# Kernel optimization log

Measured on AMD Instinct MI355X. Metric: run time of the kernel, lower is better.

## Reference

```python
import math
import jax, jax.numpy as jnp
import numpy as np

P = 8; K = 9; RC = 8; FC = 768; TOPK = 2
THR = 0.2; TEMP = 0.08; DIL = 5; MIX = 0.65; OPEN = 5


def _build_bank():
    axis = np.linspace(-1.0, 1.0, K, dtype=np.float32)
    yy, xx = np.meshgrid(axis, axis, indexing='ij')
    Ls = [0.45, 0.75, 1.05]; Ws = [0.14, 0.2, 0.28]
    kernels, oris, lens, wids = [], [], [], []
    for i in range(P):
        ang = 2.0 * math.pi * i / P
        L = Ls[i % 3]; W = Ws[(i // 3) % 3]
        xr = xx * math.cos(ang) + yy * math.sin(ang)
        yr = -xx * math.sin(ang) + yy * math.cos(ang)
        taper = (1.0 - np.clip(np.abs(xr) / L, 0.0, 1.0)) ** 1.5
        core = np.exp(-0.5 * ((xr / L) ** 2 + (yr / W) ** 2))
        ridge = taper * core * np.clip(1.0 - (yr / W) ** 2, 0.0, None)
        k = ridge - ridge.mean()
        k = k / max(np.abs(k).sum(), 1e-6)
        kernels.append(k.astype(np.float32)); oris.append(ang); lens.append(L); wids.append(W)
    return (jnp.asarray(np.stack(kernels)[:, None]),
            jnp.asarray(np.array(oris, np.float32)),
            jnp.asarray(np.array(lens, np.float32)),
            jnp.asarray(np.array(wids, np.float32)))


def _conv(x, w, b, pad):
    y = jax.lax.conv_general_dilated(x, w, (1, 1), [(pad, pad), (pad, pad)],
                                     dimension_numbers=('NCHW', 'OIHW', 'NCHW'))
    return y + b[None, :, None, None]


def _avg3(x):  # torch avg_pool2d k=3,s=1,p=1 with count_include_pad=True -> sum/9
    s = jax.lax.reduce_window(x, 0.0, jax.lax.add, (1, 1, 3, 3), (1, 1, 1, 1),
                              [(0, 0), (0, 0), (1, 1), (1, 1)])
    return s / 9.0


def _maxp(x, k):
    p = k // 2
    return jax.lax.reduce_window(x, -jnp.inf, jax.lax.max, (1, 1, k, k), (1, 1, 1, 1),
                                 [(0, 0), (0, 0), (p, p), (p, p)])


def _binary_open(mask, k):
    eroded = 1.0 - _maxp(1.0 - mask, k)
    return jnp.clip(_maxp(eroded, k), 0.0, 1.0)


def _normalize(t):
    mn = t.min(axis=(-2, -1), keepdims=True)
    mx = t.max(axis=(-2, -1), keepdims=True)
    return (t - mn) / jnp.maximum(mx - mn, 1e-6)


def _gelu(x):
    return jax.nn.gelu(x, approximate=False)


def _forward(feature_map, theta, length, width, curvature, alpha, objectness,
             prototype_logits, fp1_w, fp1_b, fp2_w, fp2_b, pm1_w, pm1_b,
             pm2_w, pm2_b, proto_delta):
    bank, ori, la, wa = _build_bank()
    carrier = _gelu(_conv(_gelu(_conv(feature_map, fp1_w, fp1_b, 0)), fp2_w, fp2_b, 1))
    carrier_mean = carrier.mean(axis=1, keepdims=True)
    carrier_hp = carrier_mean - _avg3(carrier_mean)
    kernels = bank + 0.05 * proto_delta
    responses = jax.lax.conv_general_dilated(carrier_hp, kernels, (1, 1),
                                             [(K // 2, K // 2)] * 2,
                                             dimension_numbers=('NCHW', 'OIHW', 'NCHW'))
    theta_angle = jnp.tanh(theta) * math.pi  # [B,1,H,W]
    theta_score = jnp.cos(theta_angle - ori[None, :, None, None])
    length_value = jax.nn.sigmoid(length) * 0.85 + 0.25
    width_value = jax.nn.sigmoid(width) * 0.22 + 0.08
    length_score = -(length_value - la[None, :, None, None]) ** 2 / 0.08
    width_score = -(width_value - wa[None, :, None, None]) ** 2 / 0.01
    bias = prototype_logits + 1.25 * theta_score + length_score + width_score
    pw = jax.nn.softmax(bias, axis=1)  # [B,P,H,W]
    # per-pixel top-k prototype selection
    pwt = jnp.moveaxis(pw, 1, -1)  # [B,H,W,P]
    vals, idx = jax.lax.top_k(pwt, TOPK)
    sparse = (jax.nn.one_hot(idx, P, dtype=pw.dtype) * vals[..., None]).sum(axis=-2)
    sparse = sparse / jnp.maximum(sparse.sum(axis=-1, keepdims=True), 1e-6)
    pw = jnp.moveaxis(sparse, -1, 1)
    alpha_map = jax.nn.sigmoid(alpha)
    objectness_map = jax.nn.sigmoid(objectness)
    curvature_map = jnp.tanh(curvature)
    ss = (responses * pw).sum(axis=1, keepdims=True)
    ss = ss - _avg3(ss)
    density = jnp.abs(carrier).mean(axis=1, keepdims=True)
    density = density / jnp.maximum(density.mean(axis=(2, 3), keepdims=True), 1e-6)
    dx = jnp.cos(theta_angle); dy = jnp.sin(theta_angle)
    blob = _avg3(objectness_map)
    # support gating (enabled, hard-mask + opening)
    carrier_support = _normalize(_avg3(jnp.abs(carrier_hp)))
    density_support = _normalize(density)
    ev = MIX * carrier_support + (1.0 - MIX) * density_support
    gate = jax.nn.sigmoid((ev - THR) / TEMP)
    gate = _maxp(gate, DIL)
    mask = (ev >= THR).astype(feature_map.dtype)
    mask = _binary_open(mask, OPEN)
    mask = _maxp(mask, DIL)
    gate = gate * mask
    blob = blob * jax.lax.stop_gradient(gate)
    stroke_gate = alpha_map * blob * (0.7 + 0.3 * jnp.clip(density, 0.0, 2.0))
    ss = stroke_gate * ss * (1.0 + 0.15 * curvature_map)
    feats = jnp.concatenate([carrier * ss, ss, dx * ss, dy * ss, curvature_map * ss], axis=1)  # [B,RC+4,H,W]
    h = _gelu(_conv(feats, pm1_w, pm1_b, 0))
    return _conv(h, pm2_w, pm2_b, 0)  # [B,FC,H,W]


def setup_inputs() -> dict:
    key = jax.random.key(0)
    ks = jax.random.split(key, 16)
    B, H, W = 8, 64, 64
    n = lambda k, s: jax.random.normal(k, s, dtype=jnp.float32)
    return {
        'feature_map': n(ks[0], (B, FC, H, W)),
        'theta': n(ks[1], (B, 1, H, W)),
        'length': n(ks[2], (B, 1, H, W)),
        'width': n(ks[3], (B, 1, H, W)),
        'curvature': n(ks[4], (B, 1, H, W)),
        'alpha': n(ks[5], (B, 1, H, W)),
        'objectness': n(ks[6], (B, 1, H, W)),
        'prototype_logits': n(ks[7], (B, P, H, W)),
        'fp1_w': n(ks[8], (RC, FC, 1, 1)) * 0.02,
        'fp1_b': jnp.zeros((RC,), jnp.float32),
        'fp2_w': n(ks[9], (RC, RC, 3, 3)) * 0.05,
        'fp2_b': jnp.zeros((RC,), jnp.float32),
        'pm1_w': n(ks[10], (RC, RC + 4, 1, 1)) * 0.05,
        'pm1_b': jnp.zeros((RC,), jnp.float32),
        'pm2_w': n(ks[11], (FC, RC, 1, 1)) * 0.05,
        'pm2_b': jnp.zeros((FC,), jnp.float32),
        'proto_delta': n(ks[12], (P, 1, K, K)) * 0.02,
    }


def reference(feature_map, theta, length, width, curvature, alpha, objectness,
              prototype_logits, fp1_w, fp1_b, fp2_w, fp2_b, pm1_w, pm1_b,
              pm2_w, pm2_b, proto_delta):
    return _forward(feature_map, theta, length, width, curvature, alpha, objectness,
                    prototype_logits, fp1_w, fp1_b, fp2_w, fp2_b, pm1_w, pm1_b,
                    pm2_w, pm2_b, proto_delta)
```

## Files before the change

kernel.cpp:

```cpp
#include <hip/hip_runtime.h>
#include <math.h>

#define PI_F 3.14159265358979323846f

__device__ __forceinline__ float gelu_f(float x){ return 0.5f*x*(1.0f+erff(x*0.7071067811865475f)); }
__device__ __forceinline__ float sigm_f(float x){ return 1.0f/(1.0f+expf(-x)); }


__global__ void __launch_bounds__(256) k_conv1(const float* __restrict__ fm,
                        const float* __restrict__ w1, float* __restrict__ part){
    int chunk = blockIdx.x;
    int g = blockIdx.y;
    int tid = threadIdx.x;
    __shared__ float wl[96*8];
    for (int i=tid;i<96*8;i+=256){ int c=i>>3, co=i&7; wl[i]=w1[co*768 + g*96 + c]; }
    __syncthreads();
    int b = chunk>>2;
    int q0 = ((chunk&3)<<8) + tid;
    const float4* fm4 = (const float4*)fm;
    float4 acc[8];
    #pragma unroll
    for(int co=0;co<8;co++) acc[co]=make_float4(0.f,0.f,0.f,0.f);
    int basec = b*768 + g*96;
    for(int c=0;c<96;c++){
        float4 x = fm4[(size_t)(basec+c)*1024 + q0];
        #pragma unroll
        for(int co=0;co<8;co++){
            float wv = wl[(c<<3)+co];
            acc[co].x += wv*x.x; acc[co].y += wv*x.y; acc[co].z += wv*x.z; acc[co].w += wv*x.w;
        }
    }
    float4* p4 = (float4*)part;
    int gq = (b<<10) + q0;
    #pragma unroll
    for(int co=0;co<8;co++) p4[(size_t)(g*8+co)*8192 + gq] = acc[co];
}

__global__ void __launch_bounds__(256) k_bank(const float* __restrict__ pd,
                                              float* __restrict__ klg){
    __shared__ float ridge[648];
    __shared__ float pmS[8], pdenS[8];
    int tid = threadIdx.x;
    for(int t=tid;t<648;t+=256){
        int p=t/81, idx=t-p*81;
        int i=idx/9, j=idx-i*9;
        float ay=-1.f+0.25f*(float)i;
        float ax=-1.f+0.25f*(float)j;
        float ang=2.f*PI_F*(float)p*0.125f;
        const float Ls[3]={0.45f,0.75f,1.05f};
        const float Ws[3]={0.14f,0.20f,0.28f};
        float L=Ls[p%3], Wd=Ws[(p/3)%3];
        float cs=cosf(ang), sn=sinf(ang);
        float xr=ax*cs+ay*sn;
        float yr=-ax*sn+ay*cs;
        float tp=1.f-fminf(fabsf(xr)/L,1.f);
        float taper=powf(tp,1.5f);
        float core=expf(-0.5f*((xr/L)*(xr/L)+(yr/Wd)*(yr/Wd)));
        ridge[t]=taper*core*fmaxf(1.f-(yr/Wd)*(yr/Wd),0.f);
    }
    __syncthreads();
    {
        int p=tid>>5, k=tid&31;
        float s=0.f;
        for(int e=k;e<81;e+=32) s+=ridge[p*81+e];
        for(int off=16;off>0;off>>=1) s+=__shfl_down(s,off,32);
        if(k==0) pmS[p]=s*(1.f/81.f);
    }
    __syncthreads();
    {
        int p=tid>>5, k=tid&31;
        float m=pmS[p];
        float s=0.f;
        for(int e=k;e<81;e+=32) s+=fabsf(ridge[p*81+e]-m);
        for(int off=16;off>0;off>>=1) s+=__shfl_down(s,off,32);
        if(k==0) pdenS[p]=fmaxf(s,1e-6f);
    }
    __syncthreads();
    for(int t=tid;t<648;t+=256){
        int p=t/81;
        klg[t]=(ridge[t]-pmS[p])/pdenS[p]+0.05f*pd[t];
    }
}

__global__ void __launch_bounds__(256) k_comb(float* __restrict__ part,
                                              const float* __restrict__ b1){
    int idx = blockIdx.x*256 + threadIdx.x;
    int co = idx>>13, rem = idx&8191;
    float4* p4 = (float4*)part;
    float4 s = make_float4(0.f,0.f,0.f,0.f);
    #pragma unroll
    for(int g=0;g<8;g++){
        float4 v = p4[(size_t)((g<<3)+co)*8192 + rem];
        s.x+=v.x; s.y+=v.y; s.z+=v.z; s.w+=v.w;
    }
    float bb=b1[co];
    s.x=gelu_f(s.x+bb); s.y=gelu_f(s.y+bb); s.z=gelu_f(s.z+bb); s.w=gelu_f(s.w+bb);
    p4[(size_t)co*8192 + rem] = s;
}

__global__ void __launch_bounds__(256) k_conv2(const float* __restrict__ t1,
    const float* __restrict__ w2, const float* __restrict__ b2,
    float* __restrict__ carrier, float* __restrict__ cm, float* __restrict__ absc,
    float* __restrict__ bpart){
    __shared__ float t1T[8][256];
    __shared__ float w2s[576];
    __shared__ float sumS[2][128];
    __shared__ float saS[2][128];
    __shared__ float rS[256], rMn[256], rMx[256];
    int tid=threadIdx.x, bl=blockIdx.x;
    int b=bl>>5, band=bl&31, y0=band<<1;
    for(int i=tid;i<576;i+=256) w2s[i]=w2[i];
    {
        int r=tid>>6, x=tid&63;
        int gy=y0-1+r;
        bool ok = (gy>=0 && gy<64);
        int base = (b<<12)+(gy<<6)+x;
        #pragma unroll
        for(int co=0;co<8;co++)
            t1T[co][tid] = ok ? t1[co*32768 + base] : 0.f;
    }
    __syncthreads();
    int px=tid&127, half=tid>>7;
    int ly=px>>6, x=px&63, gy=y0+ly;
    float acc[4];
    #pragma unroll
    for(int qq=0;qq<4;qq++) acc[qq]=b2[half*4+qq];
    for(int ci=0;ci<8;ci++){
        #pragma unroll
        for(int dy=-1;dy<=1;dy++){
            int tr=ly+1+dy;
            #pragma unroll
            for(int dx=-1;dx<=1;dx++){
                int xx=x+dx;
                float v=(xx>=0&&xx<64)?t1T[ci][tr*64+xx]:0.f;
                int ti=(dy+1)*3+(dx+1);
                #pragma unroll
                for(int qq=0;qq<4;qq++) acc[qq]+=v*w2s[((half*4+qq)*8+ci)*9+ti];
            }
        }
    }
    float s4=0.f, sa4=0.f;
    #pragma unroll
    for(int qq=0;qq<4;qq++){
        float cv=gelu_f(acc[qq]);
        carrier[((size_t)((b<<3)+half*4+qq)<<12)+(gy<<6)+x]=cv;
        s4+=cv; sa4+=fabsf(cv);
    }
    sumS[half][px]=s4; saS[half][px]=sa4;
    __syncthreads();
    float aS=0.f, aMn=1e30f, aMx=-1e30f;
    if(half==0){
        float cmv=(sumS[0][px]+sumS[1][px])*0.125f;
        float av =(saS[0][px]+saS[1][px])*0.125f;
        int gp=(b<<12)+(gy<<6)+x;
        cm[gp]=cmv;
        absc[gp]=av;
        aS=av; aMn=av; aMx=av;
    }
    rS[tid]=aS; rMn[tid]=aMn; rMx[tid]=aMx;
    __syncthreads();
    for(int st=128;st>0;st>>=1){
        if(tid<st){
            rS[tid]+=rS[tid+st];
            rMn[tid]=fminf(rMn[tid],rMn[tid+st]);
            rMx[tid]=fmaxf(rMx[tid],rMx[tid+st]);
        }
        __syncthreads();
    }
    if(tid==0){
        bpart[bl*8+0]=rS[0];
        bpart[bl*8+3]=rMn[0];
        bpart[bl*8+4]=rMx[0];
    }
}

__global__ void __launch_bounds__(256) k_resp(const float* __restrict__ cm,
    const float* __restrict__ klg, const float* __restrict__ theta,
    const float* __restrict__ length, const float* __restrict__ width,
    const float* __restrict__ plog,
    float* __restrict__ csraw, float* __restrict__ ss0, float* __restrict__ bpart){
    __shared__ float cmT[768];
    __shared__ float chpT[640];
    __shared__ float klS[648];
    __shared__ float mg[128][8];
    __shared__ float rMn[256], rMx[256];
    int tid=threadIdx.x, bl=blockIdx.x;
    int b=bl>>5, band=bl&31, y0=band<<1;
    for(int i=tid;i<648;i+=256) klS[i]=klg[i];
    for(int j=tid;j<768;j+=256){
        int r=j>>6, x=j&63;
        int gy=y0-5+r;
        cmT[j]=(gy>=0&&gy<64)?cm[(b<<12)+(gy<<6)+x]:0.f;
    }
    __syncthreads();
    for(int j=tid;j<640;j+=256){
        int rh=j>>6, x=j&63;
        int gy=y0-4+rh;
        float v=0.f;
        if(gy>=0&&gy<64){
            float s=0.f;
            #pragma unroll
            for(int dy=-1;dy<=1;dy++){
                #pragma unroll
                for(int dx=-1;dx<=1;dx++){
                    int xx=x+dx;
                    if(xx>=0&&xx<64) s+=cmT[(rh+1+dy)*64+xx];
                }
            }
            v=cmT[(rh+1)*64+x]-s*(1.f/9.f);
        }
        chpT[j]=v;
    }
    __syncthreads();
    int px=tid&127, half=tid>>7;
    int ly=px>>6, x=px&63, gy=y0+ly;
    int gp=(b<<12)+(gy<<6)+x;
    float acc[4];
    #pragma unroll
    for(int qq=0;qq<4;qq++) acc[qq]=0.f;
    float cs=0.f;
    for(int dy=-4;dy<=4;dy++){
        int lr=ly+dy+4;
        for(int dx=-4;dx<=4;dx++){
            int xx=x+dx;
            float v=(xx>=0&&xx<64)?chpT[lr*64+xx]:0.f;
            int ti=(dy+4)*9+(dx+4);
            #pragma unroll
            for(int qq=0;qq<4;qq++) acc[qq]+=v*klS[(half*4+qq)*81+ti];
            if(half==0 && dy>=-1&&dy<=1&&dx>=-1&&dx<=1) cs+=fabsf(v);
        }
    }
    float ta=tanhf(theta[gp])*PI_F;
    float lv=sigm_f(length[gp])*0.85f+0.25f;
    float wv=sigm_f(width[gp])*0.22f+0.08f;
    const float Ls[3]={0.45f,0.75f,1.05f};
    const float Ws[3]={0.14f,0.20f,0.28f};
    int pp=(gy<<6)+x;
    float m1=-1e30f,m2=-1e30f,r1v=0.f,r2v=0.f;
    #pragma unroll
    for(int qq=0;qq<4;qq++){
        int q=half*4+qq;
        float ang=2.f*PI_F*(float)q*0.125f;
        float la=Ls[q%3], wa=Ws[(q/3)%3];
        float bias=plog[((size_t)((b<<3)+q)<<12)+pp]
                 +1.25f*cosf(ta-ang)
                 -(lv-la)*(lv-la)*(1.f/0.08f)
                 -(wv-wa)*(wv-wa)*(1.f/0.01f);
        if(bias>m1){m2=m1;r2v=r1v;m1=bias;r1v=acc[qq];}
        else if(bias>m2){m2=bias;r2v=acc[qq];}
    }
    mg[px][half*4+0]=m1; mg[px][half*4+1]=r1v;
    mg[px][half*4+2]=m2; mg[px][half*4+3]=r2v;
    __syncthreads();
    float cMn=1e30f, cMx=-1e30f;
    if(half==0){
        float m1a=mg[px][0], r1a=mg[px][1], m2a=mg[px][2], r2a=mg[px][3];
        float m1b=mg[px][4], r1b=mg[px][5], m2b=mg[px][6], r2b=mg[px][7];
        float M1,R1,M2,R2;
        if(m1b>m1a){ M1=m1b;R1=r1b; if(m2b>m1a){M2=m2b;R2=r2b;} else {M2=m1a;R2=r1a;} }
        else       { M1=m1a;R1=r1a; if(m1b>m2a){M2=m1b;R2=r1b;} else {M2=m2a;R2=r2a;} }
        float e2=expf(M2-M1);
        float inv=1.0f/(1.0f+e2);
        ss0[gp]=R1*inv + R2*e2*inv;
        float csv=cs*(1.f/9.f);
        csraw[gp]=csv;
        cMn=csv; cMx=csv;
    }
    rMn[tid]=cMn; rMx[tid]=cMx;
    __syncthreads();
    for(int st=128;st>0;st>>=1){
        if(tid<st){
            rMn[tid]=fminf(rMn[tid],rMn[tid+st]);
            rMx[tid]=fmaxf(rMx[tid],rMx[tid+st]);
        }
        __syncthreads();
    }
    if(tid==0){
        bpart[bl*8+1]=rMn[0];
        bpart[bl*8+2]=rMx[0];
    }
}

__global__ void __launch_bounds__(1024) k_gate(const float* __restrict__ csraw,
    const float* __restrict__ absc, const float* __restrict__ objn,
    const float* __restrict__ alpha, const float* __restrict__ bpart,
    float* __restrict__ sg){
    __shared__ float A[4096], Bs[4096], Cs[4096];
    __shared__ float red5[5];
    int b=blockIdx.x, tid=threadIdx.x;
    if(tid==0){
        float sm=0.f, cmn=1e30f, cmx=-1e30f, amn=1e30f, amx=-1e30f;
        for(int j=0;j<32;j++){
            const float* bp=&bpart[(b*32+j)*8];
            sm+=bp[0];
            cmn=fminf(cmn,bp[1]); cmx=fmaxf(cmx,bp[2]);
            amn=fminf(amn,bp[3]); amx=fmaxf(amx,bp[4]);
        }
        float den=fmaxf(sm*(1.0f/4096.0f),1e-6f);
        red5[0]=den; red5[1]=cmn; red5[2]=cmx; red5[3]=amn/den; red5[4]=amx/den;
    }
    __syncthreads();
    float den=red5[0], cmn=red5[1], cmx=red5[2], dmn=red5[3], dmx=red5[4];
    float cinv = 1.0f/fmaxf(cmx-cmn,1e-6f);
    float dinv = 1.0f/fmaxf(dmx-dmn,1e-6f);
    for(int k=0;k<4;k++){
        int p=tid+k*1024;
        float cs=(csraw[(b<<12)+p]-cmn)*cinv;
        float d = absc[(b<<12)+p]/den;
        float ds=(d-dmn)*dinv;
        float ev = 0.65f*cs + 0.35f*ds;
        A[p]=ev;
        Bs[p]=sigm_f((ev-0.2f)*(1.0f/0.08f));
    }
    __syncthreads();
    for(int k=0;k<4;k++){
        int p=tid+k*1024; int y=p>>6,x=p&63;
        float m=-1e30f;
        for(int dy=-2;dy<=2;dy++){int yy=y+dy; if(yy<0||yy>=64)continue;
            for(int dx=-2;dx<=2;dx++){int xx=x+dx; if(xx<0||xx>=64)continue;
                m=fmaxf(m,Bs[(yy<<6)+xx]);}}
        Cs[p]=m;
    }
    __syncthreads();
    for(int k=0;k<4;k++){
        int p=tid+k*1024; int y=p>>6,x=p&63;
        float m=1.f;
        for(int dy=-2;dy<=2;dy++){int yy=y+dy; if(yy<0||yy>=64)continue;
            for(int dx=-2;dx<=2;dx++){int xx=x+dx; if(xx<0||xx>=64)continue;
                if (A[(yy<<6)+xx] < 0.2f) m=0.f;}}
        Bs[p]=m;
    }
    __syncthreads();
    for(int k=0;k<4;k++){
        int p=tid+k*1024; int y=p>>6,x=p&63;
        float m=-1e30f;
        for(int dy=-2;dy<=2;dy++){int yy=y+dy; if(yy<0||yy>=64)continue;
            for(int dx=-2;dx<=2;dx++){int xx=x+dx; if(xx<0||xx>=64)continue;
                m=fmaxf(m,Bs[(yy<<6)+xx]);}}
        A[p]=m;
    }
    __syncthreads();
    for(int k=0;k<4;k++){
        int p=tid+k*1024; int y=p>>6,x=p&63;
        float m=-1e30f;
        for(int dy=-2;dy<=2;dy++){int yy=y+dy; if(yy<0||yy>=64)continue;
            for(int dx=-2;dx<=2;dx++){int xx=x+dx; if(xx<0||xx>=64)continue;
                m=fmaxf(m,A[(yy<<6)+xx]);}}
        Bs[p]=m;
    }
    __syncthreads();
    for(int k=0;k<4;k++){
        int p=tid+k*1024;
        A[p]=sigm_f(objn[(b<<12)+p]);
    }
    __syncthreads();
    for(int k=0;k<4;k++){
        int p=tid+k*1024; int y=p>>6,x=p&63;
        float s=0.f;
        for(int dy=-1;dy<=1;dy++){int yy=y+dy; if(yy<0||yy>=64)continue;
            for(int dx=-1;dx<=1;dx++){int xx=x+dx; if(xx<0||xx>=64)continue;
                s += A[(yy<<6)+xx];}}
        float blob = s*(1.0f/9.0f);
        float gate = Cs[p]*Bs[p];
        float d = absc[(b<<12)+p]/den;
        float sgv = sigm_f(alpha[(b<<12)+p]) * blob * gate * (0.7f+0.3f*fminf(fmaxf(d,0.f),2.f));
        sg[(b<<12)+p] = sgv;
    }
}

__global__ void __launch_bounds__(256) k_out(const float* __restrict__ ss0,
    const float* __restrict__ sg, const float* __restrict__ theta,
    const float* __restrict__ curv, const float* __restrict__ carrier,
    const float* __restrict__ w3, const float* __restrict__ b3,
    const float* __restrict__ w4, const float* __restrict__ b4,
    float* __restrict__ out){
    __shared__ float hS[8][128];
    __shared__ float w4s[768*8];
    __shared__ float b4s[768];
    __shared__ float wl[96];
    __shared__ float bl3[8];
    int tid=threadIdx.x;
    int bln=blockIdx.x;
    for(int i=tid;i<6144;i+=256) w4s[i]=w4[i];
    for(int i=tid;i<768;i+=256) b4s[i]=b4[i];
    if(tid<96) wl[tid]=w3[tid];
    if(tid<8) bl3[tid]=b3[tid];
    __syncthreads();

    if(tid<128){
        int gp=bln*128+tid;
        int b=gp>>12, p=gp&4095, y=p>>6, x=p&63;
        const float* base = ss0 + (b<<12);
        float s=0.f;
        for(int dy=-1;dy<=1;dy++){int yy=y+dy; if(yy<0||yy>=64)continue;
            for(int dx=-1;dx<=1;dx++){int xx=x+dx;if(xx<0||xx>=64)continue;
                s+=base[(yy<<6)+xx];}}
        float ss1 = base[p]-s*(1.0f/9.0f);
        float cu = tanhf(curv[gp]);
        float ssv = sg[gp]*ss1*(1.0f+0.15f*cu);
        float ta = tanhf(theta[gp])*PI_F;
        float dxv=cosf(ta), dyv=sinf(ta);
        float car[8];
        #pragma unroll
        for(int ci=0;ci<8;ci++) car[ci]=carrier[((size_t)((b<<3)+ci)<<12)+p];
        #pragma unroll
        for(int co=0;co<8;co++){
            const float* w=&wl[co*12];
            float t = w[8] + w[9]*dxv + w[10]*dyv + w[11]*cu;
            #pragma unroll
            for(int ci=0;ci<8;ci++) t += w[ci]*car[ci];
            hS[co][tid] = gelu_f(bl3[co] + ssv*t);
        }
    }
    __syncthreads();

    int px4 = tid&31;
    int cg = tid>>5;
    int q0 = bln*32 + px4;
    int b = q0>>10;
    int ql = q0 & 1023;
    float4 hv[8];
    #pragma unroll
    for(int ci=0;ci<8;ci++) hv[ci]=*(const float4*)&hS[ci][px4<<2];
    float4* o4=(float4*)out;
    for(int k=0;k<96;k++){
        int co=cg*96+k;
        float bb=b4s[co];
        float4 o=make_float4(bb,bb,bb,bb);
        const float* w=&w4s[co<<3];
        #pragma unroll
        for(int ci=0;ci<8;ci++){
            float wv=w[ci];
            o.x+=wv*hv[ci].x; o.y+=wv*hv[ci].y; o.z+=wv*hv[ci].z; o.w+=wv*hv[ci].w;
        }
        o4[(size_t)(b*768+co)*1024 + ql]=o;
    }
}

extern "C" void kernel_launch(void* const* d_in, const int* in_sizes, int n_in,
                              void* d_out, int out_size, void* d_ws, size_t ws_size,
                              hipStream_t stream) {
    const float* fm     =(const float*)d_in[0];
    const float* theta  =(const float*)d_in[1];
    const float* length =(const float*)d_in[2];
    const float* width  =(const float*)d_in[3];
    const float* curv   =(const float*)d_in[4];
    const float* alpha  =(const float*)d_in[5];
    const float* objn   =(const float*)d_in[6];
    const float* plog   =(const float*)d_in[7];
    const float* fp1w   =(const float*)d_in[8];
    const float* fp1b   =(const float*)d_in[9];
    const float* fp2w   =(const float*)d_in[10];
    const float* fp2b   =(const float*)d_in[11];
    const float* pm1w   =(const float*)d_in[12];
    const float* pm1b   =(const float*)d_in[13];
    const float* pm2w   =(const float*)d_in[14];
    const float* pm2b   =(const float*)d_in[15];
    const float* pdelta =(const float*)d_in[16];

    float* ws=(float*)d_ws;
    float* part    = ws;
    float* t1      = part;
    float* cm      = part + 262144;
    float* carrier = part + 2097152;
    float* absc    = carrier + 262144;
    float* csraw   = absc + 32768;
    float* ss0     = csraw + 32768;
    float* sg      = ss0 + 32768;
    float* bpart   = sg + 32768;
    float* klg     = bpart + 2048;
    float* out     = (float*)d_out;

    k_bank <<<1, 256, 0, stream>>>(pdelta, klg);
    k_conv1<<<dim3(32,8), 256, 0, stream>>>(fm, fp1w, part);
    k_comb <<<256, 256, 0, stream>>>(part, fp1b);
    k_conv2<<<256, 256, 0, stream>>>(t1, fp2w, fp2b, carrier, cm, absc, bpart);
    k_resp <<<256, 256, 0, stream>>>(cm, klg, theta, length, width, plog,
                                     csraw, ss0, bpart);
    k_gate <<<8, 1024, 0, stream>>>(csraw, absc, objn, alpha, bpart, sg);
    k_out  <<<256, 256, 0, stream>>>(ss0, sg, theta, curv, carrier,
                                     pm1w, pm1b, pm2w, pm2b, out);
}
```

Before: 306.9 us.

## Fuse bank/comb into conv kernels, tile gate spatially, double grid sizes

Merges the prototype-bank kernel into conv1's first block and folds the partial-sum combine plus GELU into conv2's tile load, removing two launches and a round trip of the intermediate. conv1 now splits the channel loop across two half-blocks and reduces them in shared memory, doubling the grid. The gate kernel is retiled from 8 whole-image blocks of 1024 threads into 64 row-band blocks with halos, and the morphology chain is restructured. k_out uses half the pixels per block to double its grid. The costs are redundant halo computation, repeated partial-sum reads in conv2, and a serial bank computation appended to one conv1 block.

```diff
diff --git a/kernel.cpp b/kernel.cpp
--- a/kernel.cpp
+++ b/kernel.cpp
@@ -8,116 +8,120 @@
 
 
 __global__ void __launch_bounds__(256) k_conv1(const float* __restrict__ fm,
-                        const float* __restrict__ w1, float* __restrict__ part){
+                        const float* __restrict__ w1, const float* __restrict__ pd,
+                        float* __restrict__ part, float* __restrict__ klg){
     int chunk = blockIdx.x;
     int g = blockIdx.y;
     int tid = threadIdx.x;
     __shared__ float wl[96*8];
-    for (int i=tid;i<96*8;i+=256){ int c=i>>3, co=i&7; wl[i]=w1[co*768 + g*96 + c]; }
-    __syncthreads();
-    int b = chunk>>2;
-    int q0 = ((chunk&3)<<8) + tid;
+    __shared__ float4 comb[8][128];
+    for (int i=tid;i<768;i+=256){ int c=i>>3, co=i&7; wl[i]=w1[co*768 + g*96 + c]; }
+    __syncthreads();
+    int b = chunk>>3;
+    int f4 = tid&127, half = tid>>7;
+    int q0 = ((chunk&7)<<7) + f4;
     const float4* fm4 = (const float4*)fm;
     float4 acc[8];
     #pragma unroll
     for(int co=0;co<8;co++) acc[co]=make_float4(0.f,0.f,0.f,0.f);
-    int basec = b*768 + g*96;
-    for(int c=0;c<96;c++){
+    int basec = b*768 + g*96 + half*48;
+    for(int c=0;c<48;c++){
         float4 x = fm4[(size_t)(basec+c)*1024 + q0];
+        int ch = half*48 + c;
         #pragma unroll
         for(int co=0;co<8;co++){
-            float wv = wl[(c<<3)+co];
+            float wv = wl[(ch<<3)+co];
             acc[co].x += wv*x.x; acc[co].y += wv*x.y; acc[co].z += wv*x.z; acc[co].w += wv*x.w;
         }
     }
-    float4* p4 = (float4*)part;
-    int gq = (b<<10) + q0;
-    #pragma unroll
-    for(int co=0;co<8;co++) p4[(size_t)(g*8+co)*8192 + gq] = acc[co];
-}
-
-__global__ void __launch_bounds__(256) k_bank(const float* __restrict__ pd,
-                                              float* __restrict__ klg){
-    __shared__ float ridge[648];
-    __shared__ float pmS[8], pdenS[8];
-    int tid = threadIdx.x;
-    for(int t=tid;t<648;t+=256){
-        int p=t/81, idx=t-p*81;
-        int i=idx/9, j=idx-i*9;
-        float ay=-1.f+0.25f*(float)i;
-        float ax=-1.f+0.25f*(float)j;
-        float ang=2.f*PI_F*(float)p*0.125f;
-        const float Ls[3]={0.45f,0.75f,1.05f};
-        const float Ws[3]={0.14f,0.20f,0.28f};
-        float L=Ls[p%3], Wd=Ws[(p/3)%3];
-        float cs=cosf(ang), sn=sinf(ang);
-        float xr=ax*cs+ay*sn;
-        float yr=-ax*sn+ay*cs;
-        float tp=1.f-fminf(fabsf(xr)/L,1.f);
-        float taper=powf(tp,1.5f);
-        float core=expf(-0.5f*((xr/L)*(xr/L)+(yr/Wd)*(yr/Wd)));
-        ridge[t]=taper*core*fmaxf(1.f-(yr/Wd)*(yr/Wd),0.f);
-    }
-    __syncthreads();
-    {
-        int p=tid>>5, k=tid&31;
-        float s=0.f;
-        for(int e=k;e<81;e+=32) s+=ridge[p*81+e];
-        for(int off=16;off>0;off>>=1) s+=__shfl_down(s,off,32);
-        if(k==0) pmS[p]=s*(1.f/81.f);
-    }
-    __syncthreads();
-    {
-        int p=tid>>5, k=tid&31;
-        float m=pmS[p];
-        float s=0.f;
-        for(int e=k;e<81;e+=32) s+=fabsf(ridge[p*81+e]-m);
-        for(int off=16;off>0;off>>=1) s+=__shfl_down(s,off,32);
-        if(k==0) pdenS[p]=fmaxf(s,1e-6f);
-    }
-    __syncthreads();
-    for(int t=tid;t<648;t+=256){
-        int p=t/81;
-        klg[t]=(ridge[t]-pmS[p])/pdenS[p]+0.05f*pd[t];
-    }
-}
-
-__global__ void __launch_bounds__(256) k_comb(float* __restrict__ part,
-                                              const float* __restrict__ b1){
-    int idx = blockIdx.x*256 + threadIdx.x;
-    int co = idx>>13, rem = idx&8191;
-    float4* p4 = (float4*)part;
-    float4 s = make_float4(0.f,0.f,0.f,0.f);
-    #pragma unroll
-    for(int g=0;g<8;g++){
-        float4 v = p4[(size_t)((g<<3)+co)*8192 + rem];
-        s.x+=v.x; s.y+=v.y; s.z+=v.z; s.w+=v.w;
-    }
-    float bb=b1[co];
-    s.x=gelu_f(s.x+bb); s.y=gelu_f(s.y+bb); s.z=gelu_f(s.z+bb); s.w=gelu_f(s.w+bb);
-    p4[(size_t)co*8192 + rem] = s;
-}
-
-__global__ void __launch_bounds__(256) k_conv2(const float* __restrict__ t1,
-    const float* __restrict__ w2, const float* __restrict__ b2,
+    if(half==1){
+        #pragma unroll
+        for(int co=0;co<8;co++) comb[co][f4]=acc[co];
+    }
+    __syncthreads();
+    if(half==0){
+        float4* p4 = (float4*)part;
+        int gq = (b<<10) + q0;
+        #pragma unroll
+        for(int co=0;co<8;co++){
+            float4 o = comb[co][f4];
+            o.x+=acc[co].x; o.y+=acc[co].y; o.z+=acc[co].z; o.w+=acc[co].w;
+            p4[(size_t)((g<<3)+co)*8192 + gq] = o;
+        }
+    }
+
+    if(chunk==0 && g==0){
+        __shared__ float ridge[648];
+        __shared__ float pmS[8], pdenS[8];
+        for(int t=tid;t<648;t+=256){
+            int p=t/81, idx=t-p*81;
+            int i=idx/9, j=idx-i*9;
+            float ay=-1.f+0.25f*(float)i;
+            float ax=-1.f+0.25f*(float)j;
+            float ang=2.f*PI_F*(float)p*0.125f;
+            const float Ls[3]={0.45f,0.75f,1.05f};
+            const float Ws[3]={0.14f,0.20f,0.28f};
+            float L=Ls[p%3], Wd=Ws[(p/3)%3];
+            float cs=cosf(ang), sn=sinf(ang);
+            float xr=ax*cs+ay*sn;
+            float yr=-ax*sn+ay*cs;
+            float tp=1.f-fminf(fabsf(xr)/L,1.f);
+            float taper=powf(tp,1.5f);
+            float core=expf(-0.5f*((xr/L)*(xr/L)+(yr/Wd)*(yr/Wd)));
+            ridge[t]=taper*core*fmaxf(1.f-(yr/Wd)*(yr/Wd),0.f);
+        }
+        __syncthreads();
+        {
+            int p=tid>>5, k=tid&31;
+            float s=0.f;
+            for(int e=k;e<81;e+=32) s+=ridge[p*81+e];
+            for(int off=16;off>0;off>>=1) s+=__shfl_down(s,off,32);
+            if(k==0) pmS[p]=s*(1.f/81.f);
+        }
+        __syncthreads();
+        {
+            int p=tid>>5, k=tid&31;
+            float m=pmS[p];
+            float s=0.f;
+            for(int e=k;e<81;e+=32) s+=fabsf(ridge[p*81+e]-m);
+            for(int off=16;off>0;off>>=1) s+=__shfl_down(s,off,32);
+            if(k==0) pdenS[p]=fmaxf(s,1e-6f);
+        }
+        __syncthreads();
+        for(int t=tid;t<648;t+=256){
+            int p=t/81;
+            klg[t]=(ridge[t]-pmS[p])/pdenS[p]+0.05f*pd[t];
+        }
+    }
+}
+
+__global__ void __launch_bounds__(256) k_conv2(const float* __restrict__ part,
+    const float* __restrict__ b1, const float* __restrict__ w2, const float* __restrict__ b2,
     float* __restrict__ carrier, float* __restrict__ cm, float* __restrict__ absc,
     float* __restrict__ bpart){
     __shared__ float t1T[8][256];
     __shared__ float w2s[576];
+    __shared__ float b1s[8];
     __shared__ float sumS[2][128];
     __shared__ float saS[2][128];
     __shared__ float rS[256], rMn[256], rMx[256];
     int tid=threadIdx.x, bl=blockIdx.x;
     int b=bl>>5, band=bl&31, y0=band<<1;
     for(int i=tid;i<576;i+=256) w2s[i]=w2[i];
-    {
-        int r=tid>>6, x=tid&63;
+    if(tid<8) b1s[tid]=b1[tid];
+    __syncthreads();
+    for(int j=tid;j<2048;j+=256){
+        int co=j>>8, pos=j&255, r=pos>>6, x=pos&63;
         int gy=y0-1+r;
-        bool ok = (gy>=0 && gy<64);
-        int base = (b<<12)+(gy<<6)+x;
-        #pragma unroll
-        for(int co=0;co<8;co++)
-            t1T[co][tid] = ok ? t1[co*32768 + base] : 0.f;
+        float v=0.f;
+        if(gy>=0 && gy<64){
+            int px=(b<<12)+(gy<<6)+x;
+            float s=0.f;
+            #pragma unroll
+            for(int g=0;g<8;g++) s+=part[(size_t)((g<<3)+co)*32768+px];
+            v=gelu_f(s+b1s[co]);
+        }
+        t1T[co][pos]=v;
     }
     __syncthreads();
     int px=tid&127, half=tid>>7;
@@ -281,13 +285,18 @@
     }
 }
 
-__global__ void __launch_bounds__(1024) k_gate(const float* __restrict__ csraw,
+__global__ void __launch_bounds__(256) k_gate(const float* __restrict__ csraw,
     const float* __restrict__ absc, const float* __restrict__ objn,
     const float* __restrict__ alpha, const float* __restrict__ bpart,
     float* __restrict__ sg){
-    __shared__ float A[4096], Bs[4096], Cs[4096];
+    __shared__ float evT[1280];
+    __shared__ float gmT[1280];
+    __shared__ float eT[1024];
+    __shared__ float m1T[768];
+    __shared__ float obT[640];
     __shared__ float red5[5];
-    int b=blockIdx.x, tid=threadIdx.x;
+    int blk=blockIdx.x, tid=threadIdx.x;
+    int b=blk>>3, y0=(blk&7)<<3;
     if(tid==0){
         float sm=0.f, cmn=1e30f, cmx=-1e30f, amn=1e30f, amx=-1e30f;
         for(int j=0;j<32;j++){
@@ -300,71 +309,71 @@
         red5[0]=den; red5[1]=cmn; red5[2]=cmx; red5[3]=amn/den; red5[4]=amx/den;
     }
     __syncthreads();
-    float den=red5[0], cmn=red5[1], cmx=red5[2], dmn=red5[3], dmx=red5[4];
-    float cinv = 1.0f/fmaxf(cmx-cmn,1e-6f);
-    float dinv = 1.0f/fmaxf(dmx-dmn,1e-6f);
-    for(int k=0;k<4;k++){
-        int p=tid+k*1024;
-        float cs=(csraw[(b<<12)+p]-cmn)*cinv;
-        float d = absc[(b<<12)+p]/den;
-        float ds=(d-dmn)*dinv;
-        float ev = 0.65f*cs + 0.35f*ds;
-        A[p]=ev;
-        Bs[p]=sigm_f((ev-0.2f)*(1.0f/0.08f));
-    }
-    __syncthreads();
-    for(int k=0;k<4;k++){
-        int p=tid+k*1024; int y=p>>6,x=p&63;
-        float m=-1e30f;
-        for(int dy=-2;dy<=2;dy++){int yy=y+dy; if(yy<0||yy>=64)continue;
+    float den=red5[0], cmn=red5[1], dmn=red5[3];
+    float cinv = 1.0f/fmaxf(red5[2]-cmn,1e-6f);
+    float dinv = 1.0f/fmaxf(red5[4]-dmn,1e-6f);
+    for(int j=tid;j<1280;j+=256){
+        int r=j>>6, x=j&63; int gy=y0-6+r;
+        float ev=0.f;
+        if(gy>=0&&gy<64){
+            int gp=(b<<12)+(gy<<6)+x;
+            float cs=(csraw[gp]-cmn)*cinv;
+            float d=absc[gp]/den;
+            ev=0.65f*cs+0.35f*((d-dmn)*dinv);
+        }
+        evT[j]=ev;
+        gmT[j]=sigm_f((ev-0.2f)*(1.0f/0.08f));
+    }
+    for(int j=tid;j<640;j+=256){
+        int r=j>>6,x=j&63; int gy=y0-1+r;
+        obT[j]=(gy>=0&&gy<64)?sigm_f(objn[(b<<12)+(gy<<6)+x]):0.f;
+    }
+    __syncthreads();
+    for(int j=tid;j<1024;j+=256){
+        int r=j>>6,x=j&63; int gy=y0-4+r;
+        float m=0.f;
+        if(gy>=0&&gy<64){
+            m=1.f;
+            for(int dy=-2;dy<=2;dy++){int yy=gy+dy; if(yy<0||yy>=64)continue;
+                int lr=yy-(y0-6);
+                for(int dx=-2;dx<=2;dx++){int xx=x+dx; if(xx<0||xx>=64)continue;
+                    if(evT[(lr<<6)+xx]<0.2f) m=0.f;}}
+        }
+        eT[j]=m;
+    }
+    __syncthreads();
+    for(int j=tid;j<768;j+=256){
+        int r=j>>6,x=j&63; int gy=y0-2+r;
+        float m=0.f;
+        if(gy>=0&&gy<64){
+            m=-1e30f;
+            for(int dy=-2;dy<=2;dy++){int yy=gy+dy; if(yy<0||yy>=64)continue;
+                int lr=yy-(y0-4);
+                for(int dx=-2;dx<=2;dx++){int xx=x+dx; if(xx<0||xx>=64)continue;
+                    m=fmaxf(m,eT[(lr<<6)+xx]);}}
+        }
+        m1T[j]=m;
+    }
+    __syncthreads();
+    for(int k=0;k<2;k++){
+        int p=tid+(k<<8);
+        int ly=p>>6, x=p&63; int gy=y0+ly;
+        int gp=(b<<12)+(gy<<6)+x;
+        float m2=-1e30f, gx=-1e30f;
+        for(int dy=-2;dy<=2;dy++){int yy=gy+dy; if(yy<0||yy>=64)continue;
+            int lr1=yy-(y0-2), lr2=yy-(y0-6);
             for(int dx=-2;dx<=2;dx++){int xx=x+dx; if(xx<0||xx>=64)continue;
-                m=fmaxf(m,Bs[(yy<<6)+xx]);}}
-        Cs[p]=m;
-    }
-    __syncthreads();
-    for(int k=0;k<4;k++){
-        int p=tid+k*1024; int y=p>>6,x=p&63;
-        float m=1.f;
-        for(int dy=-2;dy<=2;dy++){int yy=y+dy; if(yy<0||yy>=64)continue;
-            for(int dx=-2;dx<=2;dx++){int xx=x+dx; if(xx<0||xx>=64)continue;
-                if (A[(yy<<6)+xx] < 0.2f) m=0.f;}}
-        Bs[p]=m;
-    }
-    __syncthreads();
-    for(int k=0;k<4;k++){
-        int p=tid+k*1024; int y=p>>6,x=p&63;
-        float m=-1e30f;
-        for(int dy=-2;dy<=2;dy++){int yy=y+dy; if(yy<0||yy>=64)continue;
-            for(int dx=-2;dx<=2;dx++){int xx=x+dx; if(xx<0||xx>=64)continue;
-                m=fmaxf(m,Bs[(yy<<6)+xx]);}}
-        A[p]=m;
-    }
-    __syncthreads();
-    for(int k=0;k<4;k++){
-        int p=tid+k*1024; int y=p>>6,x=p&63;
-        float m=-1e30f;
-        for(int dy=-2;dy<=2;dy++){int yy=y+dy; if(yy<0||yy>=64)continue;
-            for(int dx=-2;dx<=2;dx++){int xx=x+dx; if(xx<0||xx>=64)continue;
-                m=fmaxf(m,A[(yy<<6)+xx]);}}
-        Bs[p]=m;
-    }
-    __syncthreads();
-    for(int k=0;k<4;k++){
-        int p=tid+k*1024;
-        A[p]=sigm_f(objn[(b<<12)+p]);
-    }
-    __syncthreads();
-    for(int k=0;k<4;k++){
-        int p=tid+k*1024; int y=p>>6,x=p&63;
+                m2=fmaxf(m2,m1T[(lr1<<6)+xx]);
+                gx=fmaxf(gx,gmT[(lr2<<6)+xx]);}}
         float s=0.f;
-        for(int dy=-1;dy<=1;dy++){int yy=y+dy; if(yy<0||yy>=64)continue;
+        for(int dy=-1;dy<=1;dy++){int yy=gy+dy; if(yy<0||yy>=64)continue;
+            int lr=yy-(y0-1);
             for(int dx=-1;dx<=1;dx++){int xx=x+dx; if(xx<0||xx>=64)continue;
-                s += A[(yy<<6)+xx];}}
-        float blob = s*(1.0f/9.0f);
-        float gate = Cs[p]*Bs[p];
-        float d = absc[(b<<12)+p]/den;
-        float sgv = sigm_f(alpha[(b<<12)+p]) * blob * gate * (0.7f+0.3f*fminf(fmaxf(d,0.f),2.f));
-        sg[(b<<12)+p] = sgv;
+                s+=obT[(lr<<6)+xx];}}
+        float blob=s*(1.0f/9.0f);
+        float gate=gx*m2;
+        float d=absc[gp]/den;
+        sg[gp]=sigm_f(alpha[gp])*blob*gate*(0.7f+0.3f*fminf(fmaxf(d,0.f),2.f));
     }
 }
 
@@ -374,7 +383,7 @@
     const float* __restrict__ w3, const float* __restrict__ b3,
     const float* __restrict__ w4, const float* __restrict__ b4,
     float* __restrict__ out){
-    __shared__ float hS[8][128];
+    __shared__ float hS[8][64];
     __shared__ float w4s[768*8];
     __shared__ float b4s[768];
     __shared__ float wl[96];
@@ -387,8 +396,8 @@
     if(tid<8) bl3[tid]=b3[tid];
     __syncthreads();
 
-    if(tid<128){
-        int gp=bln*128+tid;
+    if(tid<64){
+        int gp=bln*64+tid;
         int b=gp>>12, p=gp&4095, y=p>>6, x=p&63;
         const float* base = ss0 + (b<<12);
         float s=0.f;
@@ -414,17 +423,17 @@
     }
     __syncthreads();
 
-    int px4 = tid&31;
-    int cg = tid>>5;
-    int q0 = bln*32 + px4;
+    int px4 = tid&15;
+    int cg = tid>>4;
+    int q0 = bln*16 + px4;
     int b = q0>>10;
     int ql = q0 & 1023;
     float4 hv[8];
     #pragma unroll
     for(int ci=0;ci<8;ci++) hv[ci]=*(const float4*)&hS[ci][px4<<2];
     float4* o4=(float4*)out;
-    for(int k=0;k<96;k++){
-        int co=cg*96+k;
+    for(int k=0;k<48;k++){
+        int co=cg*48+k;
         float bb=b4s[co];
         float4 o=make_float4(bb,bb,bb,bb);
         const float* w=&w4s[co<<3];
@@ -460,24 +469,21 @@
 
     float* ws=(float*)d_ws;
     float* part    = ws;
-    float* t1      = part;
-    float* cm      = part + 262144;
     float* carrier = part + 2097152;
     float* absc    = carrier + 262144;
     float* csraw   = absc + 32768;
     float* ss0     = csraw + 32768;
     float* sg      = ss0 + 32768;
-    float* bpart   = sg + 32768;
+    float* cm      = sg + 32768;
+    float* bpart   = cm + 32768;
     float* klg     = bpart + 2048;
     float* out     = (float*)d_out;
 
-    k_bank <<<1, 256, 0, stream>>>(pdelta, klg);
-    k_conv1<<<dim3(32,8), 256, 0, stream>>>(fm, fp1w, part);
-    k_comb <<<256, 256, 0, stream>>>(part, fp1b);
-    k_conv2<<<256, 256, 0, stream>>>(t1, fp2w, fp2b, carrier, cm, absc, bpart);
+    k_conv1<<<dim3(64,8), 256, 0, stream>>>(fm, fp1w, pdelta, part, klg);
+    k_conv2<<<256, 256, 0, stream>>>(part, fp1b, fp2w, fp2b, carrier, cm, absc, bpart);
     k_resp <<<256, 256, 0, stream>>>(cm, klg, theta, length, width, plog,
                                      csraw, ss0, bpart);
-    k_gate <<<8, 1024, 0, stream>>>(csraw, absc, objn, alpha, bpart, sg);
-    k_out  <<<256, 256, 0, stream>>>(ss0, sg, theta, curv, carrier,
+    k_gate <<<64, 256, 0, stream>>>(csraw, absc, objn, alpha, bpart, sg);
+    k_out  <<<512, 256, 0, stream>>>(ss0, sg, theta, curv, carrier,
                                      pm1w, pm1b, pm2w, pm2b, out);
 }
```

New measurement: 299.2 us. -2.5%, faster.
